# Performance work log

Hardware: AMD Instinct MI355X
Metric: run time of the kernel (lower is better)

Reference implementation:

```python
import jax, jax.numpy as jnp
import numpy as np

N = 100000      # nodes
E = 1600000     # edges (avg degree 16)
IN = 128        # in_channels
HID = 32        # hidden_channels per head
HEADS = 4
OUT = 64        # out_channels
NEG_SLOPE = 0.2 # PyG GATConv default leaky_relu slope


def setup_inputs() -> dict:
    key = jax.random.key(0)
    ks = jax.random.split(key, 12)
    def glorot(k, shape):
        fan = shape[0] + shape[-1]
        s = jnp.sqrt(6.0 / fan)
        return jax.random.uniform(k, shape, jnp.float32, -s, s)
    return {
        "x": jax.random.normal(ks[0], (N, IN), jnp.float32),
        "edge_index": jax.random.randint(ks[1], (2, E), 0, N, dtype=jnp.int64),
        # GATConv layer 1: in=IN, out=HID per head, heads=HEADS, concat=True
        "W1": glorot(ks[2], (IN, HEADS * HID)),
        "a_src1": glorot(ks[3], (HEADS, HID)),
        "a_dst1": glorot(ks[4], (HEADS, HID)),
        "b1": jnp.zeros((HEADS * HID,), jnp.float32),
        # GATConv layer 2: in=HEADS*HID, out=OUT, heads=1, concat=False
        "W2": glorot(ks[5], (HEADS * HID, OUT)),
        "a_src2": glorot(ks[6], (1, OUT)),
        "a_dst2": glorot(ks[7], (1, OUT)),
        "b2": jnp.zeros((OUT,), jnp.float32),
    }


def _gat_layer(x, src, dst, W, a_src, a_dst, bias, num_nodes, concat):
    """PyG-style GATConv (add_self_loops already applied to src/dst).
    x: [N, F_in]; src/dst: [E']; W: [F_in, H*C]; a_*: [H, C]."""
    H, C = a_src.shape
    h = (x @ W).reshape(-1, H, C)                       # [N, H, C]
    # per-node attention scores (avoid gathering full features for logits)
    e_src = (h * a_src[None]).sum(-1)                   # [N, H]
    e_dst = (h * a_dst[None]).sum(-1)                   # [N, H]
    logits = jax.nn.leaky_relu(e_src[src] + e_dst[dst], NEG_SLOPE)  # [E', H]
    # segment softmax over incoming edges of each destination node
    mx = jax.ops.segment_max(logits, dst, num_segments=num_nodes)   # [N, H]
    ex = jnp.exp(logits - mx[dst])                      # [E', H]
    den = jax.ops.segment_sum(ex, dst, num_segments=num_nodes)      # [N, H]
    alpha = ex / (den[dst] + 1e-16)                     # [E', H]
    # weighted message aggregation
    msg = h[src] * alpha[..., None]                     # [E', H, C]
    out = jax.ops.segment_sum(msg, dst, num_segments=num_nodes)     # [N, H, C]
    if concat:
        out = out.reshape(num_nodes, H * C)
    else:
        out = out.mean(axis=1)
    return out + bias


def reference(x, edge_index, W1, a_src1, a_dst1, b1, W2, a_src2, a_dst2, b2):
    n = x.shape[0]
    loops = jnp.arange(n, dtype=edge_index.dtype)
    src = jnp.concatenate([edge_index[0], loops])       # add self-loops (PyG default)
    dst = jnp.concatenate([edge_index[1], loops])
    # dropout layers are identity in eval mode
    h = _gat_layer(x, src, dst, W1, a_src1, a_dst1, b1, n, concat=True)
    h = jax.nn.elu(h)
    out = _gat_layer(h, src, dst, W2, a_src2, a_dst2, b2, n, concat=False)
    return out
```

## Files before the change

kernel.cpp:

```cpp
#include <hip/hip_runtime.h>
#include <cmath>

#define IN_F 128
#define NEG_SLOPE 0.2f
#define SEG 64
#define BSHIFT 7
#define NBMAX 1024
#define CHUNK 2048
#define SLOT 4096
#define LDSTRIDE 136

typedef short bfrag8 __attribute__((ext_vector_type(8)));
typedef float facc4 __attribute__((ext_vector_type(4)));
typedef float v2f __attribute__((ext_vector_type(2)));

__device__ __forceinline__ int ldidx(const int* ei, int pos, int is64) {
  return is64 ? ei[2 * pos] : ei[pos];
}
__device__ __forceinline__ unsigned short f2b(float f) {
  unsigned u = __float_as_uint(f);
  u += 0x7fffu + ((u >> 16) & 1u);
  return (unsigned short)(u >> 16);
}
__device__ __forceinline__ float b2f_lo(unsigned u) { return __uint_as_float(u << 16); }
__device__ __forceinline__ float b2f_hi(unsigned u) { return __uint_as_float(u & 0xffff0000u); }
__device__ __forceinline__ v2f b2f2(unsigned u) {
  v2f r; r.x = b2f_lo(u); r.y = b2f_hi(u); return r;
}
__device__ __forceinline__ void wave_lds_fence() {
  asm volatile("s_waitcnt lgkmcnt(0)" ::: "memory");
}
__device__ __forceinline__ float leaky(float l) { return fmaxf(l, NEG_SLOPE * l); }
__device__ __forceinline__ float elu(float o) { return o > 0.f ? o : __expf(o) - 1.f; }

__global__ __launch_bounds__(256) void prologue_kernel(
    const int* __restrict__ ei, int E, int* __restrict__ flag,
    int* __restrict__ bcur, int NB,
    const float* __restrict__ W1, const float* __restrict__ W2,
    unsigned short* __restrict__ Wt1g, unsigned short* __restrict__ Wt2g) {
  int b = blockIdx.x, tid = threadIdx.x;
  if (b == 0) {
    __shared__ int red[256];
    int acc = 0;
    int limit = E < 4096 ? E : 4096;
    for (int j = tid; j < limit; j += 256) acc |= ei[2 * j + 1];
    red[tid] = acc;
    __syncthreads();
    for (int s = 128; s > 0; s >>= 1) {
      if (tid < s) red[tid] |= red[tid + s];
      __syncthreads();
    }
    if (tid == 0) *flag = (red[0] == 0) ? 1 : 0;
  } else if (b == 1) {
    for (int i = tid; i < NB; i += 256) bcur[i] = i * SLOT;
  } else if (b < 8) {
    for (int i = (b - 2) * 256 + tid; i < 128 * 128; i += 6 * 256) {
      int k = i >> 7, c = i & 127;
      Wt1g[c * 128 + k] = f2b(W1[i]);
    }
  } else {
    for (int i = (b - 8) * 256 + tid; i < 128 * 64; i += 6 * 256) {
      int k = i >> 6, c = i & 63;
      Wt2g[c * 128 + k] = f2b(W2[i]);
    }
  }
}

__global__ __launch_bounds__(256) void scatter_gemm1_kernel(
    const int* __restrict__ ei, int E, int Etot, const int* __restrict__ flag,
    int NB, int nchunk, int* __restrict__ bcur, unsigned* __restrict__ ebuf,
    const float* __restrict__ x, const unsigned short* __restrict__ Wt1g,
    const float* __restrict__ asr, const float* __restrict__ ads,
    unsigned short* __restrict__ h1b, float* __restrict__ es, float* __restrict__ ed,
    int N) {
  __shared__ __align__(16) char smem[52224];
  int tid = threadIdx.x;

  if ((int)blockIdx.x < nchunk) {
    int* hcnt = (int*)smem;
    int* hcur = (int*)(smem + 4096);
    int base = blockIdx.x * CHUNK;
    int cnt = Etot - base; if (cnt > CHUNK) cnt = CHUNK;
    int is64 = *flag;
    for (int i = tid; i < NB; i += 256) hcnt[i] = 0;
    __syncthreads();
    for (int i = tid; i < cnt; i += 256) {
      int e = base + i;
      int d = (e < E) ? ldidx(ei, E + e, is64) : (e - E);
      atomicAdd(&hcnt[d >> BSHIFT], 1);
    }
    __syncthreads();
    for (int i = tid; i < NB; i += 256) {
      int c = hcnt[i];
      hcur[i] = c ? atomicAdd(&bcur[i], c) : 0;
    }
    __syncthreads();
    for (int i = tid; i < cnt; i += 256) {
      int e = base + i;
      int s, d;
      if (e < E) { s = ldidx(ei, e, is64); d = ldidx(ei, E + e, is64); }
      else       { s = e - E; d = s; }
      int pos = atomicAdd(&hcur[d >> BSHIFT], 1);
      ebuf[pos] = ((unsigned)s << 7) | ((unsigned)d & 127u);
    }
    return;
  }

  short* Wt = (short*)smem;
  short* As = (short*)(smem + 34816);
  int row0 = (blockIdx.x - nchunk) * 64;
  int lane = tid & 63, wv = tid >> 6;
  int m2 = lane & 15, quad = lane >> 4;

  for (int i = tid; i < 128 * 16; i += 256) {
    int c = i >> 4, ch = i & 15;
    *(uint4*)&Wt[c * LDSTRIDE + ch * 8] = *(const uint4*)&Wt1g[c * 128 + ch * 8];
  }
  for (int idx = tid; idx < 64 * 16; idx += 256) {
    int r = idx >> 4, ch = idx & 15;
    int n = row0 + r;
    bfrag8 sv;
    if (n < N) {
      float4 v0 = *(const float4*)&x[(size_t)n * 128 + ch * 8];
      float4 v1 = *(const float4*)&x[(size_t)n * 128 + ch * 8 + 4];
      sv[0] = (short)f2b(v0.x); sv[1] = (short)f2b(v0.y);
      sv[2] = (short)f2b(v0.z); sv[3] = (short)f2b(v0.w);
      sv[4] = (short)f2b(v1.x); sv[5] = (short)f2b(v1.y);
      sv[6] = (short)f2b(v1.z); sv[7] = (short)f2b(v1.w);
    } else {
      sv = (bfrag8)0;
    }
    *(bfrag8*)&As[r * LDSTRIDE + ch * 8] = sv;
  }
  __syncthreads();

  facc4 acc[8] = {};
  const short* Abase = &As[(wv * 16 + m2) * LDSTRIDE];
  #pragma unroll
  for (int ks = 0; ks < 4; ++ks) {
    int k = ks * 32 + quad * 8;
    bfrag8 af = *(const bfrag8*)&Abase[k];
    #pragma unroll
    for (int t = 0; t < 8; ++t) {
      bfrag8 bf = *(const bfrag8*)&Wt[(t * 16 + m2) * LDSTRIDE + k];
      acc[t] = __builtin_amdgcn_mfma_f32_16x16x32_bf16(af, bf, acc[t], 0, 0, 0);
    }
  }

  float av[8], bv[8];
  #pragma unroll
  for (int t = 0; t < 8; ++t) {
    int ai = (t >> 1) * 32 + (t & 1) * 16 + m2;
    av[t] = asr[ai]; bv[t] = ads[ai];
  }
  #pragma unroll
  for (int r = 0; r < 4; ++r) {
    int n = row0 + wv * 16 + quad * 4 + r;
    bool valid = (n < N);
    if (valid) {
      #pragma unroll
      for (int t = 0; t < 8; ++t)
        h1b[(size_t)n * 128 + t * 16 + m2] = f2b(acc[t][r]);
    }
    #pragma unroll
    for (int h = 0; h < 4; ++h) {
      float ps = acc[2 * h][r] * av[2 * h] + acc[2 * h + 1][r] * av[2 * h + 1];
      float pd = acc[2 * h][r] * bv[2 * h] + acc[2 * h + 1][r] * bv[2 * h + 1];
      ps += __shfl_xor(ps, 1); ps += __shfl_xor(ps, 2); ps += __shfl_xor(ps, 4); ps += __shfl_xor(ps, 8);
      pd += __shfl_xor(pd, 1); pd += __shfl_xor(pd, 2); pd += __shfl_xor(pd, 4); pd += __shfl_xor(pd, 8);
      if (valid && m2 == 0) {
        es[(size_t)n * 4 + h] = ps;
        ed[(size_t)n * 4 + h] = pd;
      }
    }
  }
}

__global__ __launch_bounds__(256) void bcsr_kernel(const int* __restrict__ bcur, const unsigned* __restrict__ ebuf,
                                                   int* __restrict__ rowptr, int* __restrict__ rowdeg,
                                                   int* __restrict__ csr, int N, int NB) {
  __shared__ unsigned se[SLOT];
  __shared__ int scsr[SLOT];
  __shared__ int cnt[128];
  __shared__ int cur[128];
  __shared__ int w0sum;
  int tid = threadIdx.x;
  int b = blockIdx.x;
  int lo = b * SLOT, hi = bcur[b];
  int fill = hi - lo;
  int node0 = b << BSHIFT;
  int nn = N - node0; if (nn > 128) nn = 128;
  if (tid < 128) cnt[tid] = 0;
  for (int i = tid; i < fill; i += 256) se[i] = ebuf[lo + i];
  __syncthreads();
  for (int i = tid; i < fill; i += 256) {
    atomicAdd(&cnt[se[i] & 127u], 1);
  }
  __syncthreads();
  int v = 0, incl = 0;
  if (tid < 128) {
    v = cnt[tid];
    incl = v;
    int lane = tid & 63;
    #pragma unroll
    for (int off = 1; off < 64; off <<= 1) { int t = __shfl_up(incl, off); if (lane >= off) incl += t; }
    if (tid == 63) w0sum = incl;
  }
  __syncthreads();
  if (tid < 128) {
    if (tid >= 64) incl += w0sum;
    int excl = incl - v;
    cur[tid] = excl;
    if (tid < nn) {
      rowptr[node0 + tid] = lo + excl;
      rowdeg[node0 + tid] = v;
    }
  }
  __syncthreads();
  for (int i = tid; i < fill; i += 256) {
    unsigned pr = se[i];
    int p = atomicAdd(&cur[pr & 127u], 1);
    scsr[p] = (int)(pr >> 7);
  }
  __syncthreads();
  for (int i = tid; i < fill; i += 256) csr[lo + i] = scsr[i];
}

__global__ __launch_bounds__(256) void gemm2_kernel(
    const unsigned short* __restrict__ xb, const unsigned short* __restrict__ Wt2g,
    const float* __restrict__ asr, const float* __restrict__ ads,
    unsigned short* __restrict__ h2b, float* __restrict__ es, float* __restrict__ ed,
    int N) {
  __shared__ short Wt[64 * LDSTRIDE];
  __shared__ short As[64 * LDSTRIDE];
  int tid = threadIdx.x;
  int row0 = blockIdx.x * 64;
  int lane = tid & 63, wv = tid >> 6;
  int m2 = lane & 15, quad = lane >> 4;

  for (int i = tid; i < 64 * 16; i += 256) {
    int c = i >> 4, ch = i & 15;
    *(uint4*)&Wt[c * LDSTRIDE + ch * 8] = *(const uint4*)&Wt2g[c * 128 + ch * 8];
  }
  for (int idx = tid; idx < 64 * 16; idx += 256) {
    int r = idx >> 4, ch = idx & 15;
    int n = row0 + r;
    uint4 u = (n < N) ? *(const uint4*)&xb[(size_t)n * 128 + ch * 8]
                      : make_uint4(0, 0, 0, 0);
    *(uint4*)&As[r * LDSTRIDE + ch * 8] = u;
  }
  __syncthreads();

  facc4 acc[4] = {};
  const short* Abase = &As[(wv * 16 + m2) * LDSTRIDE];
  #pragma unroll
  for (int ks = 0; ks < 4; ++ks) {
    int k = ks * 32 + quad * 8;
    bfrag8 af = *(const bfrag8*)&Abase[k];
    #pragma unroll
    for (int t = 0; t < 4; ++t) {
      bfrag8 bf = *(const bfrag8*)&Wt[(t * 16 + m2) * LDSTRIDE + k];
      acc[t] = __builtin_amdgcn_mfma_f32_16x16x32_bf16(af, bf, acc[t], 0, 0, 0);
    }
  }

  float av[4], bv[4];
  #pragma unroll
  for (int t = 0; t < 4; ++t) {
    av[t] = asr[t * 16 + m2]; bv[t] = ads[t * 16 + m2];
  }
  #pragma unroll
  for (int r = 0; r < 4; ++r) {
    int n = row0 + wv * 16 + quad * 4 + r;
    bool valid = (n < N);
    if (valid) {
      #pragma unroll
      for (int t = 0; t < 4; ++t)
        h2b[(size_t)n * 64 + t * 16 + m2] = f2b(acc[t][r]);
    }
    float ps = acc[0][r] * av[0] + acc[1][r] * av[1] + acc[2][r] * av[2] + acc[3][r] * av[3];
    float pd = acc[0][r] * bv[0] + acc[1][r] * bv[1] + acc[2][r] * bv[2] + acc[3][r] * bv[3];
    ps += __shfl_xor(ps, 1); ps += __shfl_xor(ps, 2); ps += __shfl_xor(ps, 4); ps += __shfl_xor(ps, 8);
    pd += __shfl_xor(pd, 1); pd += __shfl_xor(pd, 2); pd += __shfl_xor(pd, 4); pd += __shfl_xor(pd, 8);
    if (valid && m2 == 0) { es[n] = ps; ed[n] = pd; }
  }
}

__global__ __launch_bounds__(256) void agg1_kernel(
    const int* __restrict__ rowptr, const int* __restrict__ rowdeg, const int* __restrict__ csr,
    const float* __restrict__ es, const float* __restrict__ ed,
    const unsigned short* __restrict__ h1b, const float* __restrict__ bias1,
    unsigned short* __restrict__ hmidb, int N) {
  __shared__ float lds_a[4][4][4][SEG + 4];
  __shared__ int   lds_s[4][4][SEG + 4];
  int tid = threadIdx.x;
  int wv = tid >> 6, lane = tid & 63;
  int sub = lane >> 4, sj = lane & 15;
  int nbase = blockIdx.x * 16 + wv * 4;
  int n = nbase + sub;
  bool nvalid = (n < N);
  int start = 0, len = 0;
  if (nvalid) { start = rowptr[n]; len = rowdeg[n]; }
  int lenc = (len <= SEG) ? len : 0;

  float4 edv = nvalid ? ((const float4*)ed)[n] : make_float4(0.f, 0.f, 0.f, 0.f);
  float l[4][4];
  float mx = -1e30f;
  #pragma unroll
  for (int it = 0; it < 4; ++it) {
    int j = sj + it * 16;
    if (j < lenc) {
      int s = csr[start + j];
      lds_s[wv][sub][j] = s;
      float4 ev = ((const float4*)es)[s];
      float l0 = leaky(ev.x + edv.x);
      float l1 = leaky(ev.y + edv.y);
      float l2 = leaky(ev.z + edv.z);
      float l3 = leaky(ev.w + edv.w);
      l[it][0] = l0; l[it][1] = l1; l[it][2] = l2; l[it][3] = l3;
      mx = fmaxf(mx, fmaxf(fmaxf(l0, l1), fmaxf(l2, l3)));
    } else {
      l[it][0] = -1e30f; l[it][1] = -1e30f; l[it][2] = -1e30f; l[it][3] = -1e30f;
    }
  }
  #pragma unroll
  for (int off = 1; off < 16; off <<= 1) mx = fmaxf(mx, __shfl_xor(mx, off));

  float s0 = 0.f, s1 = 0.f, s2 = 0.f, s3 = 0.f;
  #pragma unroll
  for (int it = 0; it < 4; ++it) {
    float p0 = __expf(l[it][0] - mx);
    float p1 = __expf(l[it][1] - mx);
    float p2 = __expf(l[it][2] - mx);
    float p3 = __expf(l[it][3] - mx);
    l[it][0] = p0; l[it][1] = p1; l[it][2] = p2; l[it][3] = p3;
    s0 += p0; s1 += p1; s2 += p2; s3 += p3;
  }
  #pragma unroll
  for (int off = 1; off < 16; off <<= 1) {
    s0 += __shfl_xor(s0, off); s1 += __shfl_xor(s1, off);
    s2 += __shfl_xor(s2, off); s3 += __shfl_xor(s3, off);
  }
  float i0 = __builtin_amdgcn_rcpf(s0 + 1e-16f);
  float i1 = __builtin_amdgcn_rcpf(s1 + 1e-16f);
  float i2 = __builtin_amdgcn_rcpf(s2 + 1e-16f);
  float i3 = __builtin_amdgcn_rcpf(s3 + 1e-16f);
  #pragma unroll
  for (int it = 0; it < 4; ++it) {
    int j = sj + it * 16;
    if (j < lenc) {
      lds_a[wv][sub][0][j] = l[it][0] * i0;
      lds_a[wv][sub][1][j] = l[it][1] * i1;
      lds_a[wv][sub][2][j] = l[it][2] * i2;
      lds_a[wv][sub][3][j] = l[it][3] * i3;
    }
  }
  if (sj == 0) {
    int lenp1 = (lenc + 3) & ~3;
    for (int t = lenc; t < lenp1; ++t) {
      lds_s[wv][sub][t] = 0;
      lds_a[wv][sub][0][t] = 0.f; lds_a[wv][sub][1][t] = 0.f;
      lds_a[wv][sub][2][t] = 0.f; lds_a[wv][sub][3][t] = 0.f;
    }
  }
  wave_lds_fence();

  int fl = lane & 15, eidx = lane >> 4, hd = fl >> 2;
  const uint4* hrow = (const uint4*)h1b;
  #pragma unroll 1
  for (int i = 0; i < 4; ++i) {
    int lenC = __shfl(lenc, i << 4);
    if (lenC == 0) continue;
    int nI = nbase + i;
    const int* sP = &lds_s[wv][i][0];
    const float* aP = &lds_a[wv][i][hd][0];
    int lenp = (lenC + 3) & ~3;
    v2f C0 = {0.f, 0.f}, C1 = {0.f, 0.f}, C2 = {0.f, 0.f}, C3 = {0.f, 0.f};
    v2f D0 = {0.f, 0.f}, D1 = {0.f, 0.f}, D2 = {0.f, 0.f}, D3 = {0.f, 0.f};
    int g = 0;
    for (; g + 8 <= lenp; g += 8) {
      int sA = sP[g + eidx], sB = sP[g + 4 + eidx];
      float wA = aP[g + eidx];
      float wB = aP[g + 4 + eidx];
      uint4 uA = hrow[(size_t)sA * 16 + fl];
      uint4 uB = hrow[(size_t)sB * 16 + fl];
      v2f wA2 = {wA, wA}, wB2 = {wB, wB};
      C0 = __builtin_elementwise_fma(b2f2(uA.x), wA2, C0);
      C1 = __builtin_elementwise_fma(b2f2(uA.y), wA2, C1);
      C2 = __builtin_elementwise_fma(b2f2(uA.z), wA2, C2);
      C3 = __builtin_elementwise_fma(b2f2(uA.w), wA2, C3);
      D0 = __builtin_elementwise_fma(b2f2(uB.x), wB2, D0);
      D1 = __builtin_elementwise_fma(b2f2(uB.y), wB2, D1);
      D2 = __builtin_elementwise_fma(b2f2(uB.z), wB2, D2);
      D3 = __builtin_elementwise_fma(b2f2(uB.w), wB2, D3);
    }
    if (g < lenp) {
      int sA = sP[g + eidx];
      float wA = aP[g + eidx];
      uint4 uA = hrow[(size_t)sA * 16 + fl];
      v2f wA2 = {wA, wA};
      C0 = __builtin_elementwise_fma(b2f2(uA.x), wA2, C0);
      C1 = __builtin_elementwise_fma(b2f2(uA.y), wA2, C1);
      C2 = __builtin_elementwise_fma(b2f2(uA.z), wA2, C2);
      C3 = __builtin_elementwise_fma(b2f2(uA.w), wA2, C3);
    }
    C0 += D0; C1 += D1; C2 += D2; C3 += D3;
    float c0 = C0.x, c1 = C0.y, c2 = C1.x, c3 = C1.y;
    float c4 = C2.x, c5 = C2.y, c6 = C3.x, c7 = C3.y;
    c0 += __shfl_xor(c0, 16); c1 += __shfl_xor(c1, 16); c2 += __shfl_xor(c2, 16); c3 += __shfl_xor(c3, 16);
    c4 += __shfl_xor(c4, 16); c5 += __shfl_xor(c5, 16); c6 += __shfl_xor(c6, 16); c7 += __shfl_xor(c7, 16);
    c0 += __shfl_xor(c0, 32); c1 += __shfl_xor(c1, 32); c2 += __shfl_xor(c2, 32); c3 += __shfl_xor(c3, 32);
    c4 += __shfl_xor(c4, 32); c5 += __shfl_xor(c5, 32); c6 += __shfl_xor(c6, 32); c7 += __shfl_xor(c7, 32);
    if (eidx == 0) {
      float4 ba = *(const float4*)&bias1[fl * 8];
      float4 bb = *(const float4*)&bias1[fl * 8 + 4];
      float o0 = elu(c0 + ba.x), o1 = elu(c1 + ba.y), o2 = elu(c2 + ba.z), o3 = elu(c3 + ba.w);
      float o4 = elu(c4 + bb.x), o5 = elu(c5 + bb.y), o6 = elu(c6 + bb.z), o7 = elu(c7 + bb.w);
      uint4 pk;
      pk.x = (unsigned)f2b(o0) | ((unsigned)f2b(o1) << 16);
      pk.y = (unsigned)f2b(o2) | ((unsigned)f2b(o3) << 16);
      pk.z = (unsigned)f2b(o4) | ((unsigned)f2b(o5) << 16);
      pk.w = (unsigned)f2b(o6) | ((unsigned)f2b(o7) << 16);
      ((uint4*)hmidb)[(size_t)nI * 16 + fl] = pk;
    }
  }

  #pragma unroll 1
  for (int i = 0; i < 4; ++i) {
    int lenF = __shfl(len, i << 4);
    if (lenF <= SEG) continue;
    int stF = __shfl(start, i << 4);
    int nI = nbase + i;
    float4 ed4 = ((const float4*)ed)[nI];
    int f = lane * 2, hh = lane >> 4;
    const unsigned* h32 = (const unsigned*)h1b;
    float m0 = -1e30f, m1 = -1e30f, m2 = -1e30f, m3 = -1e30f;
    for (int j = stF + lane; j < stF + lenF; j += 64) {
      int s = csr[j];
      float4 ev = ((const float4*)es)[s];
      m0 = fmaxf(m0, leaky(ev.x + ed4.x)); m1 = fmaxf(m1, leaky(ev.y + ed4.y));
      m2 = fmaxf(m2, leaky(ev.z + ed4.z)); m3 = fmaxf(m3, leaky(ev.w + ed4.w));
    }
    #pragma unroll
    for (int off = 32; off; off >>= 1) {
      m0 = fmaxf(m0, __shfl_xor(m0, off)); m1 = fmaxf(m1, __shfl_xor(m1, off));
      m2 = fmaxf(m2, __shfl_xor(m2, off)); m3 = fmaxf(m3, __shfl_xor(m3, off));
    }
    float t0 = 0.f, t1 = 0.f, t2 = 0.f, t3 = 0.f;
    for (int j = stF + lane; j < stF + lenF; j += 64) {
      int s = csr[j];
      float4 ev = ((const float4*)es)[s];
      t0 += __expf(leaky(ev.x + ed4.x) - m0); t1 += __expf(leaky(ev.y + ed4.y) - m1);
      t2 += __expf(leaky(ev.z + ed4.z) - m2); t3 += __expf(leaky(ev.w + ed4.w) - m3);
    }
    #pragma unroll
    for (int off = 32; off; off >>= 1) {
      t0 += __shfl_xor(t0, off); t1 += __shfl_xor(t1, off);
      t2 += __shfl_xor(t2, off); t3 += __shfl_xor(t3, off);
    }
    float j0 = 1.f / (t0 + 1e-16f), j1 = 1.f / (t1 + 1e-16f);
    float j2 = 1.f / (t2 + 1e-16f), j3 = 1.f / (t3 + 1e-16f);
    float edh = (hh & 2) ? ((hh & 1) ? ed4.w : ed4.z) : ((hh & 1) ? ed4.y : ed4.x);
    float mh  = (hh & 2) ? ((hh & 1) ? m3 : m2) : ((hh & 1) ? m1 : m0);
    float ih  = (hh & 2) ? ((hh & 1) ? j3 : j2) : ((hh & 1) ? j1 : j0);
    float ax = 0.f, ay = 0.f;
    for (int j = stF; j < stF + lenF; ++j) {
      int s = csr[j];
      float lv = leaky(es[(size_t)s * 4 + hh] + edh);
      float a = __expf(lv - mh) * ih;
      unsigned u = h32[(size_t)s * 64 + lane];
      ax = fmaf(b2f_lo(u), a, ax);
      ay = fmaf(b2f_hi(u), a, ay);
    }
    float o0 = elu(ax + bias1[f]), o1 = elu(ay + bias1[f + 1]);
    unsigned packed = (unsigned)f2b(o0) | ((unsigned)f2b(o1) << 16);
    ((unsigned*)hmidb)[(size_t)nI * 64 + lane] = packed;
  }
}

__global__ __launch_bounds__(256) void agg2_kernel(
    const int* __restrict__ rowptr, const int* __restrict__ rowdeg, const int* __restrict__ csr,
    const float* __restrict__ es, const float* __restrict__ ed,
    const unsigned short* __restrict__ h2b, const float* __restrict__ bias2,
    float* __restrict__ out, int N) {
  __shared__ float lds_a[4][4][SEG + 8];
  __shared__ int   lds_s[4][4][SEG + 8];
  int tid = threadIdx.x;
  int wv = tid >> 6, lane = tid & 63;
  int sub = lane >> 4, sj = lane & 15;
  int nbase = blockIdx.x * 16 + wv * 4;
  int n = nbase + sub;
  bool nvalid = (n < N);
  int start = 0, len = 0;
  if (nvalid) { start = rowptr[n]; len = rowdeg[n]; }
  int lenc = (len <= SEG) ? len : 0;

  float edv = nvalid ? ed[n] : 0.f;
  float l[4];
  float mx = -1e30f;
  #pragma unroll
  for (int it = 0; it < 4; ++it) {
    int j = sj + it * 16;
    if (j < lenc) {
      int s = csr[start + j];
      lds_s[wv][sub][j] = s;
      float lv = leaky(es[s] + edv);
      l[it] = lv;
      mx = fmaxf(mx, lv);
    } else {
      l[it] = -1e30f;
    }
  }
  #pragma unroll
  for (int off = 1; off < 16; off <<= 1) mx = fmaxf(mx, __shfl_xor(mx, off));
  float sm = 0.f;
  #pragma unroll
  for (int it = 0; it < 4; ++it) {
    float p = __expf(l[it] - mx);
    l[it] = p;
    sm += p;
  }
  #pragma unroll
  for (int off = 1; off < 16; off <<= 1) sm += __shfl_xor(sm, off);
  float inv = __builtin_amdgcn_rcpf(sm + 1e-16f);
  #pragma unroll
  for (int it = 0; it < 4; ++it) {
    int j = sj + it * 16;
    if (j < lenc) lds_a[wv][sub][j] = l[it] * inv;
  }
  if (sj == 0) {
    int lenp1 = (lenc + 7) & ~7;
    for (int t = lenc; t < lenp1; ++t) {
      lds_s[wv][sub][t] = 0;
      lds_a[wv][sub][t] = 0.f;
    }
  }
  wave_lds_fence();

  int fl = lane & 7, eidx = lane >> 3;
  const uint4* hrow = (const uint4*)h2b;
  #pragma unroll 1
  for (int i = 0; i < 4; ++i) {
    int lenC = __shfl(lenc, i << 4);
    if (lenC == 0) continue;
    int nI = nbase + i;
    const float* aP = &lds_a[wv][i][0];
    const int*   sP = &lds_s[wv][i][0];
    int lenp = (lenC + 7) & ~7;
    v2f C0 = {0.f, 0.f}, C1 = {0.f, 0.f}, C2 = {0.f, 0.f}, C3 = {0.f, 0.f};
    v2f D0 = {0.f, 0.f}, D1 = {0.f, 0.f}, D2 = {0.f, 0.f}, D3 = {0.f, 0.f};
    int g = 0;
    for (; g + 16 <= lenp; g += 16) {
      int sA = sP[g + eidx],   sB = sP[g + 8 + eidx];
      float wA = aP[g + eidx], wB = aP[g + 8 + eidx];
      uint4 uA = hrow[(size_t)sA * 8 + fl];
      uint4 uB = hrow[(size_t)sB * 8 + fl];
      v2f wA2 = {wA, wA}, wB2 = {wB, wB};
      C0 = __builtin_elementwise_fma(b2f2(uA.x), wA2, C0);
      C1 = __builtin_elementwise_fma(b2f2(uA.y), wA2, C1);
      C2 = __builtin_elementwise_fma(b2f2(uA.z), wA2, C2);
      C3 = __builtin_elementwise_fma(b2f2(uA.w), wA2, C3);
      D0 = __builtin_elementwise_fma(b2f2(uB.x), wB2, D0);
      D1 = __builtin_elementwise_fma(b2f2(uB.y), wB2, D1);
      D2 = __builtin_elementwise_fma(b2f2(uB.z), wB2, D2);
      D3 = __builtin_elementwise_fma(b2f2(uB.w), wB2, D3);
    }
    if (g < lenp) {
      int sA = sP[g + eidx];
      float wA = aP[g + eidx];
      uint4 uA = hrow[(size_t)sA * 8 + fl];
      v2f wA2 = {wA, wA};
      C0 = __builtin_elementwise_fma(b2f2(uA.x), wA2, C0);
      C1 = __builtin_elementwise_fma(b2f2(uA.y), wA2, C1);
      C2 = __builtin_elementwise_fma(b2f2(uA.z), wA2, C2);
      C3 = __builtin_elementwise_fma(b2f2(uA.w), wA2, C3);
    }
    C0 += D0; C1 += D1; C2 += D2; C3 += D3;
    float c0 = C0.x, c1 = C0.y, c2 = C1.x, c3 = C1.y;
    float c4 = C2.x, c5 = C2.y, c6 = C3.x, c7 = C3.y;
    c0 += __shfl_xor(c0, 8);  c1 += __shfl_xor(c1, 8);  c2 += __shfl_xor(c2, 8);  c3 += __shfl_xor(c3, 8);
    c4 += __shfl_xor(c4, 8);  c5 += __shfl_xor(c5, 8);  c6 += __shfl_xor(c6, 8);  c7 += __shfl_xor(c7, 8);
    c0 += __shfl_xor(c0, 16); c1 += __shfl_xor(c1, 16); c2 += __shfl_xor(c2, 16); c3 += __shfl_xor(c3, 16);
    c4 += __shfl_xor(c4, 16); c5 += __shfl_xor(c5, 16); c6 += __shfl_xor(c6, 16); c7 += __shfl_xor(c7, 16);
    c0 += __shfl_xor(c0, 32); c1 += __shfl_xor(c1, 32); c2 += __shfl_xor(c2, 32); c3 += __shfl_xor(c3, 32);
    c4 += __shfl_xor(c4, 32); c5 += __shfl_xor(c5, 32); c6 += __shfl_xor(c6, 32); c7 += __shfl_xor(c7, 32);
    if (eidx == 0) {
      float4 ba = *(const float4*)&bias2[fl * 8];
      float4 bb = *(const float4*)&bias2[fl * 8 + 4];
      ((float4*)out)[(size_t)nI * 16 + fl * 2]     = make_float4(c0 + ba.x, c1 + ba.y, c2 + ba.z, c3 + ba.w);
      ((float4*)out)[(size_t)nI * 16 + fl * 2 + 1] = make_float4(c4 + bb.x, c5 + bb.y, c6 + bb.z, c7 + bb.w);
    }
  }

  #pragma unroll 1
  for (int i = 0; i < 4; ++i) {
    int lenF = __shfl(len, i << 4);
    if (lenF <= SEG) continue;
    int stF = __shfl(start, i << 4);
    int nI = nbase + i;
    float edF = ed[nI];
    float m = -1e30f;
    for (int j = stF + lane; j < stF + lenF; j += 64) {
      m = fmaxf(m, leaky(es[csr[j]] + edF));
    }
    #pragma unroll
    for (int off = 32; off; off >>= 1) m = fmaxf(m, __shfl_xor(m, off));
    float t = 0.f;
    for (int j = stF + lane; j < stF + lenF; j += 64) {
      t += __expf(leaky(es[csr[j]] + edF) - m);
    }
    #pragma unroll
    for (int off = 32; off; off >>= 1) t += __shfl_xor(t, off);
    float iv = 1.f / (t + 1e-16f);
    float acc = 0.f;
    for (int j = stF; j < stF + lenF; ++j) {
      int s = csr[j];
      float a = __expf(leaky(es[s] + edF) - m) * iv;
      float v = __uint_as_float(((unsigned)h2b[(size_t)s * 64 + lane]) << 16);
      acc = fmaf(v, a, acc);
    }
    out[(size_t)nI * 64 + lane] = acc + bias2[lane];
  }
}

extern "C" void kernel_launch(void* const* d_in, const int* in_sizes, int n_in,
                              void* d_out, int out_size, void* d_ws, size_t ws_size,
                              hipStream_t stream) {
  const float* x   = (const float*)d_in[0];
  const int*   ei  = (const int*)d_in[1];
  const float* W1  = (const float*)d_in[2];
  const float* as1 = (const float*)d_in[3];
  const float* ad1 = (const float*)d_in[4];
  const float* b1  = (const float*)d_in[5];
  const float* W2  = (const float*)d_in[6];
  const float* as2 = (const float*)d_in[7];
  const float* ad2 = (const float*)d_in[8];
  const float* b2  = (const float*)d_in[9];
  float* out = (float*)d_out;

  int N = in_sizes[0] / IN_F;
  int E = in_sizes[1] / 2;
  int Etot = E + N;
  int NB = (N + 127) >> BSHIFT;

  char* p = (char*)d_ws;
  auto carve = [&](size_t bytes) -> char* {
    char* r = p;
    p += (bytes + 255) & ~(size_t)255;
    return r;
  };
  int* flag     = (int*)carve(4);
  int* bcur     = (int*)carve((size_t)NBMAX * 4);
  unsigned short* Wt1g = (unsigned short*)carve(128 * 128 * 2);
  unsigned short* Wt2g = (unsigned short*)carve(64 * 128 * 2);
  unsigned* ebuf = (unsigned*)carve((size_t)NB * SLOT * 4);
  int* rowptr   = (int*)carve((size_t)(N + 1) * 4);
  int* rowdeg   = (int*)carve((size_t)(N + 1) * 4);
  int* csr      = (int*)carve((size_t)NB * SLOT * 4);
  float* es1    = (float*)carve((size_t)N * 4 * 4);
  float* ed1    = (float*)carve((size_t)N * 4 * 4);
  float* es2    = (float*)carve((size_t)N * 4);
  float* ed2    = (float*)carve((size_t)N * 4);
  unsigned short* h1b   = (unsigned short*)carve((size_t)N * 128 * 2);
  unsigned short* hmidb = (unsigned short*)carve((size_t)N * 128 * 2);
  unsigned short* h2b   = (unsigned short*)carve((size_t)N * 64 * 2);

  int nchunk = (Etot + CHUNK - 1) / CHUNK;
  int gblocks = (N + 63) / 64;
  prologue_kernel<<<14, 256, 0, stream>>>(ei, E, flag, bcur, NB, W1, W2, Wt1g, Wt2g);
  scatter_gemm1_kernel<<<nchunk + gblocks, 256, 0, stream>>>(
      ei, E, Etot, flag, NB, nchunk, bcur, ebuf,
      x, Wt1g, as1, ad1, h1b, es1, ed1, N);
  bcsr_kernel<<<NB, 256, 0, stream>>>(bcur, ebuf, rowptr, rowdeg, csr, N, NB);
  agg1_kernel<<<(N + 15) / 16, 256, 0, stream>>>(rowptr, rowdeg, csr, es1, ed1, h1b, b1, hmidb, N);
  gemm2_kernel<<<(N + 63) / 64, 256, 0, stream>>>(hmidb, Wt2g, as2, ad2, h2b, es2, ed2, N);
  agg2_kernel<<<(N + 15) / 16, 256, 0, stream>>>(rowptr, rowdeg, csr, es2, ed2, h2b, b2, out, N);
}
```

Measured before the change: 313.5 us.

## Fuse layer-2 GEMM into layer-1 aggregation kernel via LDS tile

The layer-1 aggregation kernel now keeps each block's 16 ELU outputs in shared memory instead of writing the hmid buffer to global memory. It then runs the 128x64 layer-2 projection with MFMA on that tile and computes the attention score dot products, reducing them through LDS atomics. This removes one kernel launch and a full global write and read of the intermediate features. In exchange, every block re-reads W2 from global or L2, does a small 16-row MFMA tile, and adds extra __syncthreads and LDS use that may lower occupancy.

```diff
diff --git a/kernel.cpp b/kernel.cpp
--- a/kernel.cpp
+++ b/kernel.cpp
@@ -226,82 +226,29 @@
   for (int i = tid; i < fill; i += 256) csr[lo + i] = scsr[i];
 }
 
-__global__ __launch_bounds__(256) void gemm2_kernel(
-    const unsigned short* __restrict__ xb, const unsigned short* __restrict__ Wt2g,
-    const float* __restrict__ asr, const float* __restrict__ ads,
-    unsigned short* __restrict__ h2b, float* __restrict__ es, float* __restrict__ ed,
-    int N) {
-  __shared__ short Wt[64 * LDSTRIDE];
-  __shared__ short As[64 * LDSTRIDE];
-  int tid = threadIdx.x;
-  int row0 = blockIdx.x * 64;
-  int lane = tid & 63, wv = tid >> 6;
-  int m2 = lane & 15, quad = lane >> 4;
-
-  for (int i = tid; i < 64 * 16; i += 256) {
-    int c = i >> 4, ch = i & 15;
-    *(uint4*)&Wt[c * LDSTRIDE + ch * 8] = *(const uint4*)&Wt2g[c * 128 + ch * 8];
-  }
-  for (int idx = tid; idx < 64 * 16; idx += 256) {
-    int r = idx >> 4, ch = idx & 15;
-    int n = row0 + r;
-    uint4 u = (n < N) ? *(const uint4*)&xb[(size_t)n * 128 + ch * 8]
-                      : make_uint4(0, 0, 0, 0);
-    *(uint4*)&As[r * LDSTRIDE + ch * 8] = u;
-  }
-  __syncthreads();
-
-  facc4 acc[4] = {};
-  const short* Abase = &As[(wv * 16 + m2) * LDSTRIDE];
-  #pragma unroll
-  for (int ks = 0; ks < 4; ++ks) {
-    int k = ks * 32 + quad * 8;
-    bfrag8 af = *(const bfrag8*)&Abase[k];
-    #pragma unroll
-    for (int t = 0; t < 4; ++t) {
-      bfrag8 bf = *(const bfrag8*)&Wt[(t * 16 + m2) * LDSTRIDE + k];
-      acc[t] = __builtin_amdgcn_mfma_f32_16x16x32_bf16(af, bf, acc[t], 0, 0, 0);
-    }
-  }
-
-  float av[4], bv[4];
-  #pragma unroll
-  for (int t = 0; t < 4; ++t) {
-    av[t] = asr[t * 16 + m2]; bv[t] = ads[t * 16 + m2];
-  }
-  #pragma unroll
-  for (int r = 0; r < 4; ++r) {
-    int n = row0 + wv * 16 + quad * 4 + r;
-    bool valid = (n < N);
-    if (valid) {
-      #pragma unroll
-      for (int t = 0; t < 4; ++t)
-        h2b[(size_t)n * 64 + t * 16 + m2] = f2b(acc[t][r]);
-    }
-    float ps = acc[0][r] * av[0] + acc[1][r] * av[1] + acc[2][r] * av[2] + acc[3][r] * av[3];
-    float pd = acc[0][r] * bv[0] + acc[1][r] * bv[1] + acc[2][r] * bv[2] + acc[3][r] * bv[3];
-    ps += __shfl_xor(ps, 1); ps += __shfl_xor(ps, 2); ps += __shfl_xor(ps, 4); ps += __shfl_xor(ps, 8);
-    pd += __shfl_xor(pd, 1); pd += __shfl_xor(pd, 2); pd += __shfl_xor(pd, 4); pd += __shfl_xor(pd, 8);
-    if (valid && m2 == 0) { es[n] = ps; ed[n] = pd; }
-  }
-}
-
-__global__ __launch_bounds__(256) void agg1_kernel(
+__global__ __launch_bounds__(256) void agg1_gemm2_kernel(
     const int* __restrict__ rowptr, const int* __restrict__ rowdeg, const int* __restrict__ csr,
     const float* __restrict__ es, const float* __restrict__ ed,
     const unsigned short* __restrict__ h1b, const float* __restrict__ bias1,
-    unsigned short* __restrict__ hmidb, int N) {
+    const unsigned short* __restrict__ Wt2g, const float* __restrict__ asr2, const float* __restrict__ ads2,
+    unsigned short* __restrict__ h2b, float* __restrict__ es2, float* __restrict__ ed2,
+    int N) {
   __shared__ float lds_a[4][4][4][SEG + 4];
   __shared__ int   lds_s[4][4][SEG + 4];
+  __shared__ short hm[16 * LDSTRIDE];
+  __shared__ float esp[16], edp[16];
   int tid = threadIdx.x;
   int wv = tid >> 6, lane = tid & 63;
   int sub = lane >> 4, sj = lane & 15;
-  int nbase = blockIdx.x * 16 + wv * 4;
+  int bbase = blockIdx.x * 16;
+  int nbase = bbase + wv * 4;
   int n = nbase + sub;
   bool nvalid = (n < N);
   int start = 0, len = 0;
   if (nvalid) { start = rowptr[n]; len = rowdeg[n]; }
   int lenc = (len <= SEG) ? len : 0;
+
+  if (tid < 16) { esp[tid] = 0.f; edp[tid] = 0.f; }
 
   float4 edv = nvalid ? ((const float4*)ed)[n] : make_float4(0.f, 0.f, 0.f, 0.f);
   float l[4][4];
@@ -371,7 +318,6 @@
   for (int i = 0; i < 4; ++i) {
     int lenC = __shfl(lenc, i << 4);
     if (lenC == 0) continue;
-    int nI = nbase + i;
     const int* sP = &lds_s[wv][i][0];
     const float* aP = &lds_a[wv][i][hd][0];
     int lenp = (lenC + 3) & ~3;
@@ -421,7 +367,8 @@
       pk.y = (unsigned)f2b(o2) | ((unsigned)f2b(o3) << 16);
       pk.z = (unsigned)f2b(o4) | ((unsigned)f2b(o5) << 16);
       pk.w = (unsigned)f2b(o6) | ((unsigned)f2b(o7) << 16);
-      ((uint4*)hmidb)[(size_t)nI * 16 + fl] = pk;
+      int row = wv * 4 + i;
+      *(uint4*)&hm[row * LDSTRIDE + fl * 8] = pk;
     }
   }
 
@@ -434,24 +381,24 @@
     float4 ed4 = ((const float4*)ed)[nI];
     int f = lane * 2, hh = lane >> 4;
     const unsigned* h32 = (const unsigned*)h1b;
-    float m0 = -1e30f, m1 = -1e30f, m2 = -1e30f, m3 = -1e30f;
+    float m0 = -1e30f, m1 = -1e30f, m2v = -1e30f, m3 = -1e30f;
     for (int j = stF + lane; j < stF + lenF; j += 64) {
       int s = csr[j];
       float4 ev = ((const float4*)es)[s];
       m0 = fmaxf(m0, leaky(ev.x + ed4.x)); m1 = fmaxf(m1, leaky(ev.y + ed4.y));
-      m2 = fmaxf(m2, leaky(ev.z + ed4.z)); m3 = fmaxf(m3, leaky(ev.w + ed4.w));
+      m2v = fmaxf(m2v, leaky(ev.z + ed4.z)); m3 = fmaxf(m3, leaky(ev.w + ed4.w));
     }
     #pragma unroll
     for (int off = 32; off; off >>= 1) {
       m0 = fmaxf(m0, __shfl_xor(m0, off)); m1 = fmaxf(m1, __shfl_xor(m1, off));
-      m2 = fmaxf(m2, __shfl_xor(m2, off)); m3 = fmaxf(m3, __shfl_xor(m3, off));
+      m2v = fmaxf(m2v, __shfl_xor(m2v, off)); m3 = fmaxf(m3, __shfl_xor(m3, off));
     }
     float t0 = 0.f, t1 = 0.f, t2 = 0.f, t3 = 0.f;
     for (int j = stF + lane; j < stF + lenF; j += 64) {
       int s = csr[j];
       float4 ev = ((const float4*)es)[s];
       t0 += __expf(leaky(ev.x + ed4.x) - m0); t1 += __expf(leaky(ev.y + ed4.y) - m1);
-      t2 += __expf(leaky(ev.z + ed4.z) - m2); t3 += __expf(leaky(ev.w + ed4.w) - m3);
+      t2 += __expf(leaky(ev.z + ed4.z) - m2v); t3 += __expf(leaky(ev.w + ed4.w) - m3);
     }
     #pragma unroll
     for (int off = 32; off; off >>= 1) {
@@ -461,7 +408,7 @@
     float j0 = 1.f / (t0 + 1e-16f), j1 = 1.f / (t1 + 1e-16f);
     float j2 = 1.f / (t2 + 1e-16f), j3 = 1.f / (t3 + 1e-16f);
     float edh = (hh & 2) ? ((hh & 1) ? ed4.w : ed4.z) : ((hh & 1) ? ed4.y : ed4.x);
-    float mh  = (hh & 2) ? ((hh & 1) ? m3 : m2) : ((hh & 1) ? m1 : m0);
+    float mh  = (hh & 2) ? ((hh & 1) ? m3 : m2v) : ((hh & 1) ? m1 : m0);
     float ih  = (hh & 2) ? ((hh & 1) ? j3 : j2) : ((hh & 1) ? j1 : j0);
     float ax = 0.f, ay = 0.f;
     for (int j = stF; j < stF + lenF; ++j) {
@@ -474,7 +421,39 @@
     }
     float o0 = elu(ax + bias1[f]), o1 = elu(ay + bias1[f + 1]);
     unsigned packed = (unsigned)f2b(o0) | ((unsigned)f2b(o1) << 16);
-    ((unsigned*)hmidb)[(size_t)nI * 64 + lane] = packed;
+    int row = wv * 4 + i;
+    *(unsigned*)&hm[row * LDSTRIDE + lane * 2] = packed;
+  }
+
+  __syncthreads();
+
+  facc4 acc2 = {};
+  #pragma unroll
+  for (int ks = 0; ks < 4; ++ks) {
+    int k = ks * 32 + sub * 8;
+    bfrag8 af = *(const bfrag8*)&hm[sj * LDSTRIDE + k];
+    bfrag8 bf = *(const bfrag8*)&Wt2g[(size_t)(wv * 16 + sj) * 128 + k];
+    acc2 = __builtin_amdgcn_mfma_f32_16x16x32_bf16(af, bf, acc2, 0, 0, 0);
+  }
+  float a2 = asr2[wv * 16 + sj], b2v = ads2[wv * 16 + sj];
+  #pragma unroll
+  for (int r = 0; r < 4; ++r) {
+    int row = sub * 4 + r;
+    int nO = bbase + row;
+    if (nO < N) h2b[(size_t)nO * 64 + wv * 16 + sj] = f2b(acc2[r]);
+    float ps = acc2[r] * a2;
+    float pd = acc2[r] * b2v;
+    ps += __shfl_xor(ps, 1); ps += __shfl_xor(ps, 2); ps += __shfl_xor(ps, 4); ps += __shfl_xor(ps, 8);
+    pd += __shfl_xor(pd, 1); pd += __shfl_xor(pd, 2); pd += __shfl_xor(pd, 4); pd += __shfl_xor(pd, 8);
+    if (sj == 0) {
+      atomicAdd(&esp[row], ps);
+      atomicAdd(&edp[row], pd);
+    }
+  }
+  __syncthreads();
+  if (tid < 16) {
+    int nO = bbase + tid;
+    if (nO < N) { es2[nO] = esp[tid]; ed2[nO] = edp[tid]; }
   }
 }
 
@@ -662,7 +641,6 @@
   float* es2    = (float*)carve((size_t)N * 4);
   float* ed2    = (float*)carve((size_t)N * 4);
   unsigned short* h1b   = (unsigned short*)carve((size_t)N * 128 * 2);
-  unsigned short* hmidb = (unsigned short*)carve((size_t)N * 128 * 2);
   unsigned short* h2b   = (unsigned short*)carve((size_t)N * 64 * 2);
 
   int nchunk = (Etot + CHUNK - 1) / CHUNK;
@@ -672,7 +650,8 @@
       ei, E, Etot, flag, NB, nchunk, bcur, ebuf,
       x, Wt1g, as1, ad1, h1b, es1, ed1, N);
   bcsr_kernel<<<NB, 256, 0, stream>>>(bcur, ebuf, rowptr, rowdeg, csr, N, NB);
-  agg1_kernel<<<(N + 15) / 16, 256, 0, stream>>>(rowptr, rowdeg, csr, es1, ed1, h1b, b1, hmidb, N);
-  gemm2_kernel<<<(N + 63) / 64, 256, 0, stream>>>(hmidb, Wt2g, as2, ad2, h2b, es2, ed2, N);
+  agg1_gemm2_kernel<<<(N + 15) / 16, 256, 0, stream>>>(
+      rowptr, rowdeg, csr, es1, ed1, h1b, b1,
+      Wt2g, as2, ad2, h2b, es2, ed2, N);
   agg2_kernel<<<(N + 15) / 16, 256, 0, stream>>>(rowptr, rowdeg, csr, es2, ed2, h2b, b2, out, N);
 }
```

After: 323.9 us. 3.3% more time.
